# Performance work log

Hardware: AMD Instinct MI355X
Metric: run time of the kernel (lower is better)

## Reference

```python
import jax, jax.numpy as jnp
import numpy as np

N = 30000
NUM_FEAT = 129   # data.x.shape[1] + 1
NUM_CLASSES = 40
HID = 64

def _gat_conv(x, src, dst, W, a_src, a_dst, bias):
    """PyG GATConv (concat=True, negative_slope=0.2), self-loops pre-added to src/dst."""
    n = x.shape[0]
    H, C = a_src.shape
    h = (x @ W).reshape(n, H, C)                       # [N,H,C]
    alpha_s = jnp.sum(h * a_src[None], axis=-1)        # [N,H]
    alpha_d = jnp.sum(h * a_dst[None], axis=-1)        # [N,H]
    e = jax.nn.leaky_relu(alpha_s[src] + alpha_d[dst], 0.2)   # [E,H]
    m = jax.ops.segment_max(e, dst, num_segments=n)
    m = jnp.where(jnp.isfinite(m), m, 0.0)
    ex = jnp.exp(e - m[dst])
    denom = jax.ops.segment_sum(ex, dst, num_segments=n)
    alpha = ex / (denom[dst] + 1e-16)                  # segment softmax over in-edges
    out = jax.ops.segment_sum(h[src] * alpha[:, :, None], dst, num_segments=n)
    return out.reshape(n, H * C) + bias


def setup_inputs() -> dict:
    key = jax.random.key(0)
    ks = jax.random.split(key, 16)
    E = 480000
    x = jax.random.normal(ks[0], (N, NUM_FEAT), dtype=jnp.float32)
    edge_index = jax.random.randint(ks[1], (2, E), 0, N, dtype=jnp.int64)
    def w(k, shape, fan_in):
        return (jax.random.normal(k, shape, dtype=jnp.float32) * (1.0 / np.sqrt(fan_in))).astype(jnp.float32)
    # conv1: in=129, H=7, C=64
    W1 = w(ks[2], (NUM_FEAT, 7 * HID), NUM_FEAT)
    a1s = w(ks[3], (7, HID), HID); a1d = w(ks[4], (7, HID), HID)
    b1 = jnp.zeros((7 * HID,), jnp.float32)
    # conv2: in=448, H=6, C=64
    W2 = w(ks[5], (7 * HID, 6 * HID), 7 * HID)
    a2s = w(ks[6], (6, HID), HID); a2d = w(ks[7], (6, HID), HID)
    b2 = jnp.zeros((6 * HID,), jnp.float32)
    # conv3: in=384, H=6, C=40
    W3 = w(ks[8], (6 * HID, 6 * NUM_CLASSES), 6 * HID)
    a3s = w(ks[9], (6, NUM_CLASSES), NUM_CLASSES); a3d = w(ks[10], (6, NUM_CLASSES), NUM_CLASSES)
    b3 = jnp.zeros((6 * NUM_CLASSES,), jnp.float32)
    return {"x": x, "edge_index": edge_index,
            "W1": W1, "a1s": a1s, "a1d": a1d, "b1": b1,
            "W2": W2, "a2s": a2s, "a2d": a2d, "b2": b2,
            "W3": W3, "a3s": a3s, "a3d": a3d, "b3": b3}


def reference(x, edge_index, W1, a1s, a1d, b1, W2, a2s, a2d, b2, W3, a3s, a3d, b3):
    n = x.shape[0]
    loop = jnp.arange(n, dtype=edge_index.dtype)
    src = jnp.concatenate([edge_index[0], loop])   # PyG add_self_loops=True
    dst = jnp.concatenate([edge_index[1], loop])
    # dropout is identity in eval mode
    h = _gat_conv(x, src, dst, W1, a1s, a1d, b1)
    h = jax.nn.relu(h)
    h = _gat_conv(h, src, dst, W2, a2s, a2d, b2)
    h = jax.nn.relu(h)
    out = _gat_conv(h, src, dst, W3, a3s, a3d, b3)
    return out
```

## Files before the change

kernel.cpp:

```cpp
#include <hip/hip_runtime.h>
#include <hip/hip_bf16.h>


#define NFEAT 129
#define MPAD  30080
#define BLKSH 11
#define KPD   16

typedef __attribute__((ext_vector_type(8))) short short8v;
typedef __attribute__((ext_vector_type(8))) unsigned short u16x8;
typedef __attribute__((ext_vector_type(8))) __bf16 bf16x8;
typedef __attribute__((ext_vector_type(4))) float f32x4;
typedef unsigned short u16;

union FragU { short8v s; bf16x8 b; };

__device__ inline u16 f2bf(float x) {
    unsigned u = __builtin_bit_cast(unsigned, x);
    unsigned r = (u + 0x7fffu + ((u >> 16) & 1u)) >> 16;
    return (u16)r;
}
__device__ inline float bf2f(u16 b) {
    unsigned u = ((unsigned)b) << 16;
    return __builtin_bit_cast(float, u);
}
__device__ inline float h2f(u16 u) { return (float)__builtin_bit_cast(_Float16, u); }
__device__ inline u16 f2h(float v) { return __builtin_bit_cast(u16, (_Float16)v); }


__global__ __launch_bounds__(256) void hist_k(const int* __restrict__ src,
                                              const int* __restrict__ dst,
                                              int* __restrict__ cnt, int E, int n) {
    int e = blockIdx.x * 256 + threadIdx.x;
    if (e < E + n) {
        int s, d;
        if (e < E) { s = src[e]; d = dst[e]; }
        else       { s = d = e - E; }
        atomicAdd(&cnt[d * KPD + (s >> BLKSH)], 1);
    }
}

__global__ __launch_bounds__(256) void bsum_k(const int* __restrict__ cnt,
                                              int* __restrict__ bsum, int nk) {
    __shared__ int sh[256];
    int t = threadIdx.x, idx = blockIdx.x * 256 + t;
    sh[t] = (idx < nk) ? cnt[idx] : 0;
    __syncthreads();
    for (int o = 128; o; o >>= 1) {
        if (t < o) sh[t] += sh[t + o];
        __syncthreads();
    }
    if (t == 0) bsum[blockIdx.x] = sh[0];
}

__global__ __launch_bounds__(1024) void bscan_k(const int* __restrict__ bsum,
                                                int* __restrict__ bofs, int nb) {
    __shared__ int part[1024];
    int t = threadIdx.x;
    int per = (nb + 1023) >> 10;
    int base = t * per;
    int s = 0;
    for (int j = 0; j < per; ++j) {
        int i = base + j;
        if (i < nb) s += bsum[i];
    }
    part[t] = s;
    __syncthreads();
    for (int o = 1; o < 1024; o <<= 1) {
        int v = 0;
        if (t >= o) v = part[t - o];
        __syncthreads();
        if (t >= o) part[t] += v;
        __syncthreads();
    }
    int run = (t > 0) ? part[t - 1] : 0;
    for (int j = 0; j < per; ++j) {
        int i = base + j;
        if (i < nb) { bofs[i] = run; run += bsum[i]; }
    }
    if (t == 1023) bofs[nb] = part[1023];
}

__global__ __launch_bounds__(256) void scanw_k(const int* __restrict__ cnt,
                                               const int* __restrict__ bofs,
                                               int* __restrict__ row_ptr, int nk) {
    __shared__ int sh[256];
    int t = threadIdx.x, idx = blockIdx.x * 256 + t;
    int v = (idx < nk) ? cnt[idx] : 0;
    sh[t] = v;
    __syncthreads();
    for (int o = 1; o < 256; o <<= 1) {
        int u = 0;
        if (t >= o) u = sh[t - o];
        __syncthreads();
        if (t >= o) sh[t] += u;
        __syncthreads();
    }
    if (idx < nk) row_ptr[idx] = bofs[blockIdx.x] + sh[t] - v;
    if (idx == nk - 1) row_ptr[nk] = bofs[blockIdx.x] + sh[t];
}

__global__ __launch_bounds__(256) void scatter_k(const int* __restrict__ src, const int* __restrict__ dst,
                                                 const int* __restrict__ row_ptr, int* __restrict__ fill,
                                                 int* __restrict__ col, int E, int n) {
    int e = blockIdx.x * 256 + threadIdx.x;
    if (e < E + n) {
        int s, d;
        if (e < E) { s = src[e]; d = dst[e]; }
        else       { s = d = e - E; }
        int key = d * KPD + (s >> BLKSH);
        int pos = row_ptr[key] + atomicAdd(&fill[key], 1);
        col[pos] = s;
    }
}


__global__ __launch_bounds__(256) void xsplit_k(const float* __restrict__ in,
                                                u16* __restrict__ hi, u16* __restrict__ lo,
                                                int Nn, int K, int Kp, int Mp) {
    int idx = blockIdx.x * 256 + threadIdx.x;
    if (idx >= Mp * Kp) return;
    int m = idx / Kp, k = idx - m * Kp;
    float v = (m < Nn && k < K) ? in[(size_t)m * K + k] : 0.f;
    u16 h = f2bf(v);
    hi[idx] = h;
    lo[idx] = f2bf(v - bf2f(h));
}


__global__ __launch_bounds__(256) void wsplitAll_k(const float* __restrict__ W1,
                                                   const float* __restrict__ W2,
                                                   const float* __restrict__ W3,
                                                   u16* __restrict__ hi, u16* __restrict__ lo) {
    int idx = blockIdx.x * 256 + threadIdx.x;
    if (idx >= 352256) return;
    const float* W; int loc, Kp, K, N;
    if (idx < 81920)       { W = W1; loc = idx;          Kp = 160; K = 129; N = 448; }
    else if (idx < 253952) { W = W2; loc = idx - 81920;  Kp = 448; K = 448; N = 384; }
    else                   { W = W3; loc = idx - 253952; Kp = 384; K = 384; N = 240; }
    int nn = loc / Kp, k = loc - nn * Kp;
    float v = (k < K && nn < N) ? W[(size_t)k * N + nn] : 0.f;
    u16 h = f2bf(v);
    hi[idx] = h;
    lo[idx] = f2bf(v - bf2f(h));
}


__global__ __launch_bounds__(256) void projAll_k(
    const float* __restrict__ W1, const float* __restrict__ a1s, const float* __restrict__ a1d,
    const float* __restrict__ W2, const float* __restrict__ a2s, const float* __restrict__ a2d,
    const float* __restrict__ W3, const float* __restrict__ a3s, const float* __restrict__ a3d,
    float* __restrict__ Ps, float* __restrict__ Pd) {
    int idx = blockIdx.x * 256 + threadIdx.x;
    if (idx >= 992 * 8) return;
    int row = idx >> 3, h = idx & 7;
    const float *W, *as_, *ad_; int k, K, Ncols, H, C;
    if (row < 160)      { k = row;       K = 129; W = W1; as_ = a1s; ad_ = a1d; Ncols = 448; H = 7; C = 64; }
    else if (row < 608) { k = row - 160; K = 448; W = W2; as_ = a2s; ad_ = a2d; Ncols = 384; H = 6; C = 64; }
    else                { k = row - 608; K = 384; W = W3; as_ = a3s; ad_ = a3d; Ncols = 240; H = 6; C = 40; }
    float ps = 0.f, pd = 0.f;
    if (h < H && k < K) {
        const float* wr = W + (size_t)k * Ncols + h * C;
        const float* ar = as_ + h * C;
        const float* dr = ad_ + h * C;
        for (int c = 0; c < C; ++c) {
            float wv = wr[c];
            ps += wv * ar[c];
            pd += wv * dr[c];
        }
    }
    Ps[idx] = ps;
    Pd[idx] = pd;
}


__global__ __launch_bounds__(256) void zeropads_k(u16* __restrict__ h1hi, u16* __restrict__ h1lo,
                                                  int Nn) {
    int tot = (MPAD - Nn) * 448;
    int idx = blockIdx.x * 256 + threadIdx.x;
    if (idx < tot) {
        h1hi[(size_t)Nn * 448 + idx] = 0;
        h1lo[(size_t)Nn * 448 + idx] = 0;
    }
}


__global__ __launch_bounds__(256) void alpha1_k(const float* __restrict__ x,
                                                const float* __restrict__ Ps,
                                                const float* __restrict__ Pd,
                                                float* __restrict__ oS, float* __restrict__ oD, int n) {
    int wv = threadIdx.x >> 6, lane = threadIdx.x & 63;
    int i = blockIdx.x * 4 + wv;
    if (i >= n) return;
    const float* row = x + (size_t)i * NFEAT;
    float x0 = row[lane], x1 = row[64 + lane];
    float ps[8], pd[8];
    #pragma unroll
    for (int h = 0; h < 8; ++h) {
        ps[h] = x0 * Ps[lane * 8 + h] + x1 * Ps[(64 + lane) * 8 + h];
        pd[h] = x0 * Pd[lane * 8 + h] + x1 * Pd[(64 + lane) * 8 + h];
    }
    if (lane == 0) {
        float x2 = row[128];
        #pragma unroll
        for (int h = 0; h < 8; ++h) {
            ps[h] += x2 * Ps[128 * 8 + h];
            pd[h] += x2 * Pd[128 * 8 + h];
        }
    }
    #pragma unroll
    for (int h = 0; h < 8; ++h) {
        #pragma unroll
        for (int off = 32; off; off >>= 1) {
            ps[h] += __shfl_xor(ps[h], off);
            pd[h] += __shfl_xor(pd[h], off);
        }
    }
    if (lane == 0) {
        #pragma unroll
        for (int h = 0; h < 8; ++h) {
            oS[(size_t)i * 8 + h] = ps[h];
            oD[(size_t)i * 8 + h] = pd[h];
        }
    }
}


__device__ __forceinline__ int swz(int r, int s) {
    return (r << 2) | ((s ^ (r & 3) ^ ((r >> 2) & 3)) & 3);
}


__global__ __launch_bounds__(256) void gemm16(
    const u16* __restrict__ Ahi, const u16* __restrict__ Alo,
    const u16* __restrict__ Bhi, const u16* __restrict__ Blo,
    u16* __restrict__ C16, int M, int Ncols, int Kp)
{
    __shared__ __align__(16) u16 sAh[128 * 32];
    __shared__ __align__(16) u16 sAl[128 * 32];
    __shared__ __align__(16) u16 sBh[128 * 32];
    __shared__ __align__(16) u16 sBl[128 * 32];
    const int tid = threadIdx.x;
    const int m0 = blockIdx.y * 128;
    const int n0 = blockIdx.x * 128;
    const int lane = tid & 63, wave = tid >> 6;
    const int wm = wave >> 1, wn = wave & 1;
    const int l15 = lane & 15, lg = lane >> 4;
    const int r0 = tid >> 2, s0 = tid & 3;
    const int w0 = swz(r0, s0), w1 = swz(r0 + 64, s0);
    f32x4 acc[4][4] = {};

    for (int k0 = 0; k0 < Kp; k0 += 32) {
        size_t gA0 = (size_t)(m0 + r0) * Kp + k0 + s0 * 8;
        size_t gA1 = (size_t)(m0 + r0 + 64) * Kp + k0 + s0 * 8;
        size_t gB0 = (size_t)(n0 + r0) * Kp + k0 + s0 * 8;
        size_t gB1 = (size_t)(n0 + r0 + 64) * Kp + k0 + s0 * 8;
        short8v ah0 = *(const short8v*)(Ahi + gA0);
        short8v ah1 = *(const short8v*)(Ahi + gA1);
        short8v al0 = *(const short8v*)(Alo + gA0);
        short8v al1 = *(const short8v*)(Alo + gA1);
        short8v bh0 = *(const short8v*)(Bhi + gB0);
        short8v bh1 = *(const short8v*)(Bhi + gB1);
        short8v bl0 = *(const short8v*)(Blo + gB0);
        short8v bl1 = *(const short8v*)(Blo + gB1);
        __syncthreads();
        ((short8v*)sAh)[w0] = ah0; ((short8v*)sAh)[w1] = ah1;
        ((short8v*)sAl)[w0] = al0; ((short8v*)sAl)[w1] = al1;
        ((short8v*)sBh)[w0] = bh0; ((short8v*)sBh)[w1] = bh1;
        ((short8v*)sBl)[w0] = bl0; ((short8v*)sBl)[w1] = bl1;
        __syncthreads();
        FragU fah[4], fal[4], fbh[4], fbl[4];
        #pragma unroll
        for (int mf = 0; mf < 4; ++mf) {
            int rr = wm * 64 + mf * 16 + l15;
            int idx = swz(rr, lg);
            fah[mf].s = ((const short8v*)sAh)[idx];
            fal[mf].s = ((const short8v*)sAl)[idx];
        }
        #pragma unroll
        for (int nf = 0; nf < 4; ++nf) {
            int rr = wn * 64 + nf * 16 + l15;
            int idx = swz(rr, lg);
            fbh[nf].s = ((const short8v*)sBh)[idx];
            fbl[nf].s = ((const short8v*)sBl)[idx];
        }
        #pragma unroll
        for (int mf = 0; mf < 4; ++mf) {
            #pragma unroll
            for (int nf = 0; nf < 4; ++nf) {
                acc[mf][nf] = __builtin_amdgcn_mfma_f32_16x16x32_bf16(fah[mf].b, fbh[nf].b, acc[mf][nf], 0, 0, 0);
                acc[mf][nf] = __builtin_amdgcn_mfma_f32_16x16x32_bf16(fah[mf].b, fbl[nf].b, acc[mf][nf], 0, 0, 0);
                acc[mf][nf] = __builtin_amdgcn_mfma_f32_16x16x32_bf16(fal[mf].b, fbh[nf].b, acc[mf][nf], 0, 0, 0);
            }
        }
    }
    #pragma unroll
    for (int mf = 0; mf < 4; ++mf) {
        #pragma unroll
        for (int nf = 0; nf < 4; ++nf) {
            int colg = n0 + wn * 64 + nf * 16 + l15;
            if (colg >= Ncols) continue;
            #pragma unroll
            for (int r = 0; r < 4; ++r) {
                int rowg = m0 + wm * 64 + mf * 16 + lg * 4 + r;
                if (rowg < M) C16[(size_t)rowg * Ncols + colg] = f2h(acc[mf][nf][r]);
            }
        }
    }
}


template <int H, int C, bool RELU, bool SPLIT, bool PROJ>
__global__ __launch_bounds__(256) void aggF_k(
    const u16* __restrict__ hf,
    const float* __restrict__ as_, const float* __restrict__ ad_,
    const float* __restrict__ bias,
    const int* __restrict__ row_ptr,
    const int* __restrict__ col,
    const float* __restrict__ Pns, const float* __restrict__ Pnd,
    float* __restrict__ nas, float* __restrict__ nad,
    float* __restrict__ outf, u16* __restrict__ ohi, u16* __restrict__ olo,
    int n)
{
    constexpr int HC = H * C;
    constexpr int LACT = HC / 8;
    const int wv = threadIdx.x >> 6, lane = threadIdx.x & 63;
    const int i = blockIdx.x * 4 + wv;
    if (i >= n) return;
    const int ch0 = lane * 8;
    const bool act = lane < LACT;
    const int h = act ? (ch0 / C) : 0;
    const bool lead = act && ((ch0 % C) == 0);
    const int beg = row_ptr[i * KPD], end = row_ptr[(i + 1) * KPD];
    float acc[8] = {};
    float dp = 0.f;
    if (act) {
        const float adh = ad_[(size_t)i * 8 + h];
        int e = beg;
        for (; e + 4 <= end; e += 4) {
            int sA = col[e],     sB = col[e + 1];
            int sC = col[e + 2], sD = col[e + 3];
            float fA = as_[(size_t)sA * 8 + h] + adh;
            float fB = as_[(size_t)sB * 8 + h] + adh;
            float fC = as_[(size_t)sC * 8 + h] + adh;
            float fD = as_[(size_t)sD * 8 + h] + adh;
            u16x8 vA = *(const u16x8*)(hf + (size_t)sA * HC + ch0);
            u16x8 vB = *(const u16x8*)(hf + (size_t)sB * HC + ch0);
            u16x8 vC = *(const u16x8*)(hf + (size_t)sC * HC + ch0);
            u16x8 vD = *(const u16x8*)(hf + (size_t)sD * HC + ch0);
            fA = fA > 0.f ? fA : 0.2f * fA;
            fB = fB > 0.f ? fB : 0.2f * fB;
            fC = fC > 0.f ? fC : 0.2f * fC;
            fD = fD > 0.f ? fD : 0.2f * fD;
            float wA = __expf(fA), wB = __expf(fB);
            float wC = __expf(fC), wD = __expf(fD);
            #pragma unroll
            for (int j = 0; j < 8; ++j)
                acc[j] += wA * h2f(vA[j]) + wB * h2f(vB[j])
                        + wC * h2f(vC[j]) + wD * h2f(vD[j]);
            if (lead) dp += (wA + wB) + (wC + wD);
        }
        for (; e + 2 <= end; e += 2) {
            int sA = col[e], sB = col[e + 1];
            float fA = as_[(size_t)sA * 8 + h] + adh;
            float fB = as_[(size_t)sB * 8 + h] + adh;
            u16x8 vA = *(const u16x8*)(hf + (size_t)sA * HC + ch0);
            u16x8 vB = *(const u16x8*)(hf + (size_t)sB * HC + ch0);
            fA = fA > 0.f ? fA : 0.2f * fA;
            fB = fB > 0.f ? fB : 0.2f * fB;
            float wA = __expf(fA), wB = __expf(fB);
            #pragma unroll
            for (int j = 0; j < 8; ++j)
                acc[j] += wA * h2f(vA[j]) + wB * h2f(vB[j]);
            if (lead) dp += wA + wB;
        }
        if (e < end) {
            int sA = col[e];
            float fA = as_[(size_t)sA * 8 + h] + adh;
            u16x8 vA = *(const u16x8*)(hf + (size_t)sA * HC + ch0);
            fA = fA > 0.f ? fA : 0.2f * fA;
            float wA = __expf(fA);
            #pragma unroll
            for (int j = 0; j < 8; ++j)
                acc[j] += wA * h2f(vA[j]);
            if (lead) dp += wA;
        }
    }
    const float den = __shfl(dp, h * (C / 8)) + 1e-16f;
    float o[8];
    #pragma unroll
    for (int j = 0; j < 8; ++j) o[j] = 0.f;
    if (act) {
        #pragma unroll
        for (int j = 0; j < 8; ++j) {
            float v = acc[j] / den + bias[ch0 + j];
            if (RELU) v = fmaxf(v, 0.f);
            o[j] = v;
        }
        size_t base = (size_t)i * HC + ch0;
        if constexpr (SPLIT) {
            u16x8 ph, pl;
            #pragma unroll
            for (int j = 0; j < 8; ++j) {
                u16 hi = f2bf(o[j]);
                ph[j] = hi;
                pl[j] = f2bf(o[j] - bf2f(hi));
            }
            *(u16x8*)(ohi + base) = ph;
            *(u16x8*)(olo + base) = pl;
        } else {
            float4 q0; q0.x = o[0]; q0.y = o[1]; q0.z = o[2]; q0.w = o[3];
            float4 q1; q1.x = o[4]; q1.y = o[5]; q1.z = o[6]; q1.w = o[7];
            *(float4*)(outf + base) = q0;
            *(float4*)(outf + base + 4) = q1;
        }
    }
    if constexpr (PROJ) {
        float ps[8] = {}, pd[8] = {};
        if (act) {
            #pragma unroll
            for (int j = 0; j < 8; ++j) {
                const float* prs = Pns + (size_t)(ch0 + j) * 8;
                const float* prd = Pnd + (size_t)(ch0 + j) * 8;
                #pragma unroll
                for (int hp = 0; hp < 8; ++hp) {
                    ps[hp] += o[j] * prs[hp];
                    pd[hp] += o[j] * prd[hp];
                }
            }
        }
        #pragma unroll
        for (int hp = 0; hp < 8; ++hp) {
            #pragma unroll
            for (int off = 32; off; off >>= 1) {
                ps[hp] += __shfl_xor(ps[hp], off);
                pd[hp] += __shfl_xor(pd[hp], off);
            }
        }
        if (lane == 0) {
            #pragma unroll
            for (int hp = 0; hp < 8; ++hp) {
                nas[(size_t)i * 8 + hp] = ps[hp];
                nad[(size_t)i * 8 + hp] = pd[hp];
            }
        }
    }
}


extern "C" void kernel_launch(void* const* d_in, const int* in_sizes, int n_in,
                              void* d_out, int out_size, void* d_ws, size_t ws_size,
                              hipStream_t stream) {
    const float* x   = (const float*)d_in[0];
    const int*   ei  = (const int*)d_in[1];
    const float* W1  = (const float*)d_in[2];
    const float* a1s = (const float*)d_in[3];
    const float* a1d = (const float*)d_in[4];
    const float* b1  = (const float*)d_in[5];
    const float* W2  = (const float*)d_in[6];
    const float* a2s = (const float*)d_in[7];
    const float* a2d = (const float*)d_in[8];
    const float* b2  = (const float*)d_in[9];
    const float* W3  = (const float*)d_in[10];
    const float* a3s = (const float*)d_in[11];
    const float* a3d = (const float*)d_in[12];
    const float* b3  = (const float*)d_in[13];
    float* out = (float*)d_out;

    const int Nn = in_sizes[0] / NFEAT;
    const int E  = in_sizes[1] / 2;
    const int Et = E + Nn;
    const int NK = Nn * KPD;
    const int NB = (NK + 255) / 256;
    const int* srcp = ei;
    const int* dstp = ei + E;

    char* ws = (char*)d_ws;
    size_t off = 0;
    auto carve = [&](size_t bytes) -> char* {
        char* p = ws + off;
        off += (bytes + 255) & ~(size_t)255;
        return p;
    };
    u16*   hbuf16 = (u16*)carve((size_t)MPAD * 448 * 2);
    u16*   h1hi  = (u16*)carve((size_t)MPAD * 448 * 2);
    u16*   h1lo  = (u16*)carve((size_t)MPAD * 448 * 2);
    u16*   Xhi   = (u16*)carve((size_t)MPAD * 160 * 2);
    u16*   Xlo   = (u16*)carve((size_t)MPAD * 160 * 2);
    u16*   Wthi  = (u16*)carve((size_t)352256 * 2);
    u16*   Wtlo  = (u16*)carve((size_t)352256 * 2);
    int*   col   = (int*)carve((size_t)Et * 4);
    int* row_ptr = (int*)carve((size_t)(NK + 1) * 4);
    int*   cnt   = (int*)carve((size_t)NK * 4);
    int*   bsum  = (int*)carve((size_t)NB * 4);
    int*   bofs  = (int*)carve((size_t)(NB + 1) * 4);
    float* aA    = (float*)carve((size_t)Nn * 8 * 4);
    float* dA    = (float*)carve((size_t)Nn * 8 * 4);
    float* aB    = (float*)carve((size_t)Nn * 8 * 4);
    float* dB    = (float*)carve((size_t)Nn * 8 * 4);
    float* Ps    = (float*)carve((size_t)992 * 8 * 4);
    float* Pd    = (float*)carve((size_t)992 * 8 * 4);
    (void)ws_size;

    const int nb4 = (Nn + 3) / 4;
    const int mg  = MPAD / 128;

    hipMemsetAsync(cnt, 0, (size_t)NK * 4, stream);
    hist_k<<<(Et + 255) / 256, 256, 0, stream>>>(srcp, dstp, cnt, E, Nn);
    bsum_k<<<NB, 256, 0, stream>>>(cnt, bsum, NK);
    bscan_k<<<1, 1024, 0, stream>>>(bsum, bofs, NB);
    scanw_k<<<NB, 256, 0, stream>>>(cnt, bofs, row_ptr, NK);
    hipMemsetAsync(cnt, 0, (size_t)NK * 4, stream);
    scatter_k<<<(Et + 255) / 256, 256, 0, stream>>>(srcp, dstp, row_ptr, cnt, col, E, Nn);

    xsplit_k<<<((MPAD * 160) + 255) / 256, 256, 0, stream>>>(x, Xhi, Xlo, Nn, NFEAT, 160, MPAD);
    wsplitAll_k<<<(352256 + 255) / 256, 256, 0, stream>>>(W1, W2, W3, Wthi, Wtlo);
    projAll_k<<<(992 * 8 + 255) / 256, 256, 0, stream>>>(W1, a1s, a1d, W2, a2s, a2d, W3, a3s, a3d, Ps, Pd);
    zeropads_k<<<(((MPAD - Nn) * 448) + 255) / 256, 256, 0, stream>>>(h1hi, h1lo, Nn);

    alpha1_k<<<nb4, 256, 0, stream>>>(x, Ps, Pd, aA, dA, Nn);
    gemm16<<<dim3(4, mg), 256, 0, stream>>>(Xhi, Xlo, Wthi, Wtlo, hbuf16, Nn, 448, 160);
    aggF_k<7, 64, true, true, true><<<nb4, 256, 0, stream>>>(
        hbuf16, aA, dA, b1, row_ptr, col, Ps + 1280, Pd + 1280, aB, dB,
        nullptr, h1hi, h1lo, Nn);

    gemm16<<<dim3(3, mg), 256, 0, stream>>>(h1hi, h1lo, Wthi + 81920, Wtlo + 81920, hbuf16, Nn, 384, 448);
    aggF_k<6, 64, true, true, true><<<nb4, 256, 0, stream>>>(
        hbuf16, aB, dB, b2, row_ptr, col, Ps + 4864, Pd + 4864, aA, dA,
        nullptr, h1hi, h1lo, Nn);

    gemm16<<<dim3(2, mg), 256, 0, stream>>>(h1hi, h1lo, Wthi + 253952, Wtlo + 253952, hbuf16, Nn, 240, 384);
    aggF_k<6, 40, false, false, false><<<nb4, 256, 0, stream>>>(
        hbuf16, aA, dA, b3, row_ptr, col, nullptr, nullptr, nullptr, nullptr,
        out, nullptr, nullptr, Nn);
}
```

Baseline: 557.7 us.

## Precompute edge weights, store fp32 features, and split aggregation across channel blocks

Adds a per-edge kernel that computes exp(leaky_relu(alpha_s+alpha_d)) for every edge and head into a buffer, using a destination array recorded during the CSR scatter. The GEMM now writes fp32 instead of fp16, and the aggregation reads float4 features over a 2D grid split by channel block. The next layer's attention projection moves out of the aggregation into a separate kernel. This removes redundant exp and gather work per channel lane, but doubles feature gather bytes and adds extra kernels and buffer traffic.

```diff
diff --git a/kernel.cpp b/kernel.cpp
--- a/kernel.cpp
+++ b/kernel.cpp
@@ -24,8 +24,6 @@
     unsigned u = ((unsigned)b) << 16;
     return __builtin_bit_cast(float, u);
 }
-__device__ inline float h2f(u16 u) { return (float)__builtin_bit_cast(_Float16, u); }
-__device__ inline u16 f2h(float v) { return __builtin_bit_cast(u16, (_Float16)v); }
 
 
 __global__ __launch_bounds__(256) void hist_k(const int* __restrict__ src,
@@ -102,7 +100,8 @@
 
 __global__ __launch_bounds__(256) void scatter_k(const int* __restrict__ src, const int* __restrict__ dst,
                                                  const int* __restrict__ row_ptr, int* __restrict__ fill,
-                                                 int* __restrict__ col, int E, int n) {
+                                                 int* __restrict__ col, int* __restrict__ dstc,
+                                                 int E, int n) {
     int e = blockIdx.x * 256 + threadIdx.x;
     if (e < E + n) {
         int s, d;
@@ -111,6 +110,7 @@
         int key = d * KPD + (s >> BLKSH);
         int pos = row_ptr[key] + atomicAdd(&fill[key], 1);
         col[pos] = s;
+        dstc[pos] = d;
     }
 }
 
@@ -226,15 +226,71 @@
 }
 
 
+template <int KC>
+__global__ __launch_bounds__(256) void alphaproj_k(const u16* __restrict__ Hhi,
+                                                   const u16* __restrict__ Hlo,
+                                                   const float* __restrict__ Ps,
+                                                   const float* __restrict__ Pd,
+                                                   float* __restrict__ oS, float* __restrict__ oD, int n) {
+    constexpr int STRIDE = KC * 64;
+    int wv = threadIdx.x >> 6, lane = threadIdx.x & 63;
+    int i = blockIdx.x * 4 + wv;
+    if (i >= n) return;
+    const u16* bh = Hhi + (size_t)i * STRIDE;
+    const u16* bl = Hlo + (size_t)i * STRIDE;
+    float ps[8] = {}, pd[8] = {};
+    #pragma unroll
+    for (int kc = 0; kc < KC; ++kc) {
+        int k = kc * 64 + lane;
+        float v = bf2f(bh[k]) + bf2f(bl[k]);
+        #pragma unroll
+        for (int h = 0; h < 8; ++h) {
+            ps[h] += v * Ps[k * 8 + h];
+            pd[h] += v * Pd[k * 8 + h];
+        }
+    }
+    #pragma unroll
+    for (int h = 0; h < 8; ++h) {
+        #pragma unroll
+        for (int off = 32; off; off >>= 1) {
+            ps[h] += __shfl_xor(ps[h], off);
+            pd[h] += __shfl_xor(pd[h], off);
+        }
+    }
+    if (lane == 0) {
+        #pragma unroll
+        for (int h = 0; h < 8; ++h) {
+            oS[(size_t)i * 8 + h] = ps[h];
+            oD[(size_t)i * 8 + h] = pd[h];
+        }
+    }
+}
+
+
+__global__ __launch_bounds__(256) void edgew_k(const float* __restrict__ as_,
+                                               const float* __restrict__ ad_,
+                                               const int* __restrict__ col,
+                                               const int* __restrict__ dstc,
+                                               float* __restrict__ w, int Et) {
+    int idx = blockIdx.x * 256 + threadIdx.x;
+    if (idx >= Et * 8) return;
+    int e = idx >> 3, h = idx & 7;
+    int s = col[e], d = dstc[e];
+    float v = as_[(size_t)s * 8 + h] + ad_[(size_t)d * 8 + h];
+    v = v > 0.f ? v : 0.2f * v;
+    w[idx] = __expf(v);
+}
+
+
 __device__ __forceinline__ int swz(int r, int s) {
     return (r << 2) | ((s ^ (r & 3) ^ ((r >> 2) & 3)) & 3);
 }
 
 
-__global__ __launch_bounds__(256) void gemm16(
+__global__ __launch_bounds__(256) void gemm32(
     const u16* __restrict__ Ahi, const u16* __restrict__ Alo,
     const u16* __restrict__ Bhi, const u16* __restrict__ Blo,
-    u16* __restrict__ C16, int M, int Ncols, int Kp)
+    float* __restrict__ C, int M, int Ncols, int Kp)
 {
     __shared__ __align__(16) u16 sAh[128 * 32];
     __shared__ __align__(16) u16 sAl[128 * 32];
@@ -303,146 +359,76 @@
             #pragma unroll
             for (int r = 0; r < 4; ++r) {
                 int rowg = m0 + wm * 64 + mf * 16 + lg * 4 + r;
-                if (rowg < M) C16[(size_t)rowg * Ncols + colg] = f2h(acc[mf][nf][r]);
+                if (rowg < M) C[(size_t)rowg * Ncols + colg] = acc[mf][nf][r];
             }
         }
     }
 }
 
 
-template <int H, int C, bool RELU, bool SPLIT, bool PROJ>
-__global__ __launch_bounds__(256) void aggF_k(
-    const u16* __restrict__ hf,
-    const float* __restrict__ as_, const float* __restrict__ ad_,
+template <int H, int C, int CPB, bool RELU, bool SPLIT>
+__global__ __launch_bounds__(256) void gat_agg4(
+    const float* __restrict__ hfeat, const float* __restrict__ w,
     const float* __restrict__ bias,
-    const int* __restrict__ row_ptr,
-    const int* __restrict__ col,
-    const float* __restrict__ Pns, const float* __restrict__ Pnd,
-    float* __restrict__ nas, float* __restrict__ nad,
-    float* __restrict__ outf, u16* __restrict__ ohi, u16* __restrict__ olo,
-    int n)
+    const int* __restrict__ row_ptr, const int* __restrict__ col,
+    float* __restrict__ outf, u16* __restrict__ ohi, u16* __restrict__ olo, int n)
 {
     constexpr int HC = H * C;
-    constexpr int LACT = HC / 8;
     const int wv = threadIdx.x >> 6, lane = threadIdx.x & 63;
     const int i = blockIdx.x * 4 + wv;
     if (i >= n) return;
-    const int ch0 = lane * 8;
-    const bool act = lane < LACT;
-    const int h = act ? (ch0 / C) : 0;
-    const bool lead = act && ((ch0 % C) == 0);
+    const int ch = blockIdx.y * CPB + lane * 4;
+    const bool act = (lane * 4 < CPB) && (ch < HC);
+    const int h = act ? (ch / C) : 0;
+    const int cinh = act ? (ch % C) : 0;
     const int beg = row_ptr[i * KPD], end = row_ptr[(i + 1) * KPD];
-    float acc[8] = {};
-    float dp = 0.f;
+    float a0 = 0.f, a1 = 0.f, a2 = 0.f, a3 = 0.f, dp = 0.f;
     if (act) {
-        const float adh = ad_[(size_t)i * 8 + h];
+        const bool lead = (cinh == 0);
         int e = beg;
-        for (; e + 4 <= end; e += 4) {
-            int sA = col[e],     sB = col[e + 1];
-            int sC = col[e + 2], sD = col[e + 3];
-            float fA = as_[(size_t)sA * 8 + h] + adh;
-            float fB = as_[(size_t)sB * 8 + h] + adh;
-            float fC = as_[(size_t)sC * 8 + h] + adh;
-            float fD = as_[(size_t)sD * 8 + h] + adh;
-            u16x8 vA = *(const u16x8*)(hf + (size_t)sA * HC + ch0);
-            u16x8 vB = *(const u16x8*)(hf + (size_t)sB * HC + ch0);
-            u16x8 vC = *(const u16x8*)(hf + (size_t)sC * HC + ch0);
-            u16x8 vD = *(const u16x8*)(hf + (size_t)sD * HC + ch0);
-            fA = fA > 0.f ? fA : 0.2f * fA;
-            fB = fB > 0.f ? fB : 0.2f * fB;
-            fC = fC > 0.f ? fC : 0.2f * fC;
-            fD = fD > 0.f ? fD : 0.2f * fD;
-            float wA = __expf(fA), wB = __expf(fB);
-            float wC = __expf(fC), wD = __expf(fD);
-            #pragma unroll
-            for (int j = 0; j < 8; ++j)
-                acc[j] += wA * h2f(vA[j]) + wB * h2f(vB[j])
-                        + wC * h2f(vC[j]) + wD * h2f(vD[j]);
-            if (lead) dp += (wA + wB) + (wC + wD);
-        }
         for (; e + 2 <= end; e += 2) {
             int sA = col[e], sB = col[e + 1];
-            float fA = as_[(size_t)sA * 8 + h] + adh;
-            float fB = as_[(size_t)sB * 8 + h] + adh;
-            u16x8 vA = *(const u16x8*)(hf + (size_t)sA * HC + ch0);
-            u16x8 vB = *(const u16x8*)(hf + (size_t)sB * HC + ch0);
-            fA = fA > 0.f ? fA : 0.2f * fA;
-            fB = fB > 0.f ? fB : 0.2f * fB;
-            float wA = __expf(fA), wB = __expf(fB);
-            #pragma unroll
-            for (int j = 0; j < 8; ++j)
-                acc[j] += wA * h2f(vA[j]) + wB * h2f(vB[j]);
+            float wA = w[(size_t)e * 8 + h];
+            float wB = w[(size_t)(e + 1) * 8 + h];
+            float4 hA = *(const float4*)(hfeat + (size_t)sA * HC + ch);
+            float4 hB = *(const float4*)(hfeat + (size_t)sB * HC + ch);
+            a0 += wA * hA.x + wB * hB.x;
+            a1 += wA * hA.y + wB * hB.y;
+            a2 += wA * hA.z + wB * hB.z;
+            a3 += wA * hA.w + wB * hB.w;
             if (lead) dp += wA + wB;
         }
         if (e < end) {
             int sA = col[e];
-            float fA = as_[(size_t)sA * 8 + h] + adh;
-            u16x8 vA = *(const u16x8*)(hf + (size_t)sA * HC + ch0);
-            fA = fA > 0.f ? fA : 0.2f * fA;
-            float wA = __expf(fA);
-            #pragma unroll
-            for (int j = 0; j < 8; ++j)
-                acc[j] += wA * h2f(vA[j]);
+            float wA = w[(size_t)e * 8 + h];
+            float4 hA = *(const float4*)(hfeat + (size_t)sA * HC + ch);
+            a0 += wA * hA.x; a1 += wA * hA.y; a2 += wA * hA.z; a3 += wA * hA.w;
             if (lead) dp += wA;
         }
     }
-    const float den = __shfl(dp, h * (C / 8)) + 1e-16f;
-    float o[8];
-    #pragma unroll
-    for (int j = 0; j < 8; ++j) o[j] = 0.f;
+    const float den = __shfl(dp, lane - (cinh >> 2)) + 1e-16f;
     if (act) {
-        #pragma unroll
-        for (int j = 0; j < 8; ++j) {
-            float v = acc[j] / den + bias[ch0 + j];
-            if (RELU) v = fmaxf(v, 0.f);
-            o[j] = v;
-        }
-        size_t base = (size_t)i * HC + ch0;
+        const float4 b4 = *(const float4*)(bias + ch);
+        float o0 = a0 / den + b4.x;
+        float o1 = a1 / den + b4.y;
+        float o2 = a2 / den + b4.z;
+        float o3 = a3 / den + b4.w;
+        if (RELU) {
+            o0 = fmaxf(o0, 0.f); o1 = fmaxf(o1, 0.f);
+            o2 = fmaxf(o2, 0.f); o3 = fmaxf(o3, 0.f);
+        }
+        size_t base = (size_t)i * HC + ch;
         if constexpr (SPLIT) {
-            u16x8 ph, pl;
-            #pragma unroll
-            for (int j = 0; j < 8; ++j) {
-                u16 hi = f2bf(o[j]);
-                ph[j] = hi;
-                pl[j] = f2bf(o[j] - bf2f(hi));
-            }
-            *(u16x8*)(ohi + base) = ph;
-            *(u16x8*)(olo + base) = pl;
+            ushort4 ph, pl;
+            ph.x = f2bf(o0); pl.x = f2bf(o0 - bf2f(ph.x));
+            ph.y = f2bf(o1); pl.y = f2bf(o1 - bf2f(ph.y));
+            ph.z = f2bf(o2); pl.z = f2bf(o2 - bf2f(ph.z));
+            ph.w = f2bf(o3); pl.w = f2bf(o3 - bf2f(ph.w));
+            *(ushort4*)(ohi + base) = ph;
+            *(ushort4*)(olo + base) = pl;
         } else {
-            float4 q0; q0.x = o[0]; q0.y = o[1]; q0.z = o[2]; q0.w = o[3];
-            float4 q1; q1.x = o[4]; q1.y = o[5]; q1.z = o[6]; q1.w = o[7];
-            *(float4*)(outf + base) = q0;
-            *(float4*)(outf + base + 4) = q1;
-        }
-    }
-    if constexpr (PROJ) {
-        float ps[8] = {}, pd[8] = {};
-        if (act) {
-            #pragma unroll
-            for (int j = 0; j < 8; ++j) {
-                const float* prs = Pns + (size_t)(ch0 + j) * 8;
-                const float* prd = Pnd + (size_t)(ch0 + j) * 8;
-                #pragma unroll
-                for (int hp = 0; hp < 8; ++hp) {
-                    ps[hp] += o[j] * prs[hp];
-                    pd[hp] += o[j] * prd[hp];
-                }
-            }
-        }
-        #pragma unroll
-        for (int hp = 0; hp < 8; ++hp) {
-            #pragma unroll
-            for (int off = 32; off; off >>= 1) {
-                ps[hp] += __shfl_xor(ps[hp], off);
-                pd[hp] += __shfl_xor(pd[hp], off);
-            }
-        }
-        if (lane == 0) {
-            #pragma unroll
-            for (int hp = 0; hp < 8; ++hp) {
-                nas[(size_t)i * 8 + hp] = ps[hp];
-                nad[(size_t)i * 8 + hp] = pd[hp];
-            }
+            float4 o; o.x = o0; o.y = o1; o.z = o2; o.w = o3;
+            *(float4*)(outf + base) = o;
         }
     }
 }
@@ -482,14 +468,16 @@
         off += (bytes + 255) & ~(size_t)255;
         return p;
     };
-    u16*   hbuf16 = (u16*)carve((size_t)MPAD * 448 * 2);
+    float* hbuf  = (float*)carve((size_t)MPAD * 448 * 4);
     u16*   h1hi  = (u16*)carve((size_t)MPAD * 448 * 2);
     u16*   h1lo  = (u16*)carve((size_t)MPAD * 448 * 2);
     u16*   Xhi   = (u16*)carve((size_t)MPAD * 160 * 2);
     u16*   Xlo   = (u16*)carve((size_t)MPAD * 160 * 2);
     u16*   Wthi  = (u16*)carve((size_t)352256 * 2);
     u16*   Wtlo  = (u16*)carve((size_t)352256 * 2);
+    float* wbuf  = (float*)carve((size_t)Et * 8 * 4);
     int*   col   = (int*)carve((size_t)Et * 4);
+    int*   dstc  = (int*)carve((size_t)Et * 4);
     int* row_ptr = (int*)carve((size_t)(NK + 1) * 4);
     int*   cnt   = (int*)carve((size_t)NK * 4);
     int*   bsum  = (int*)carve((size_t)NB * 4);
@@ -511,7 +499,7 @@
     bscan_k<<<1, 1024, 0, stream>>>(bsum, bofs, NB);
     scanw_k<<<NB, 256, 0, stream>>>(cnt, bofs, row_ptr, NK);
     hipMemsetAsync(cnt, 0, (size_t)NK * 4, stream);
-    scatter_k<<<(Et + 255) / 256, 256, 0, stream>>>(srcp, dstp, row_ptr, cnt, col, E, Nn);
+    scatter_k<<<(Et + 255) / 256, 256, 0, stream>>>(srcp, dstp, row_ptr, cnt, col, dstc, E, Nn);
 
     xsplit_k<<<((MPAD * 160) + 255) / 256, 256, 0, stream>>>(x, Xhi, Xlo, Nn, NFEAT, 160, MPAD);
     wsplitAll_k<<<(352256 + 255) / 256, 256, 0, stream>>>(W1, W2, W3, Wthi, Wtlo);
@@ -519,18 +507,20 @@
     zeropads_k<<<(((MPAD - Nn) * 448) + 255) / 256, 256, 0, stream>>>(h1hi, h1lo, Nn);
 
     alpha1_k<<<nb4, 256, 0, stream>>>(x, Ps, Pd, aA, dA, Nn);
-    gemm16<<<dim3(4, mg), 256, 0, stream>>>(Xhi, Xlo, Wthi, Wtlo, hbuf16, Nn, 448, 160);
-    aggF_k<7, 64, true, true, true><<<nb4, 256, 0, stream>>>(
-        hbuf16, aA, dA, b1, row_ptr, col, Ps + 1280, Pd + 1280, aB, dB,
-        nullptr, h1hi, h1lo, Nn);
-
-    gemm16<<<dim3(3, mg), 256, 0, stream>>>(h1hi, h1lo, Wthi + 81920, Wtlo + 81920, hbuf16, Nn, 384, 448);
-    aggF_k<6, 64, true, true, true><<<nb4, 256, 0, stream>>>(
-        hbuf16, aB, dB, b2, row_ptr, col, Ps + 4864, Pd + 4864, aA, dA,
-        nullptr, h1hi, h1lo, Nn);
-
-    gemm16<<<dim3(2, mg), 256, 0, stream>>>(h1hi, h1lo, Wthi + 253952, Wtlo + 253952, hbuf16, Nn, 240, 384);
-    aggF_k<6, 40, false, false, false><<<nb4, 256, 0, stream>>>(
-        hbuf16, aA, dA, b3, row_ptr, col, nullptr, nullptr, nullptr, nullptr,
-        out, nullptr, nullptr, Nn);
-}
+    edgew_k<<<(Et * 8 + 255) / 256, 256, 0, stream>>>(aA, dA, col, dstc, wbuf, Et);
+    gemm32<<<dim3(4, mg), 256, 0, stream>>>(Xhi, Xlo, Wthi, Wtlo, hbuf, Nn, 448, 160);
+    gat_agg4<7, 64, 256, true, true><<<dim3(nb4, 2), 256, 0, stream>>>(
+        hbuf, wbuf, b1, row_ptr, col, nullptr, h1hi, h1lo, Nn);
+    alphaproj_k<7><<<nb4, 256, 0, stream>>>(h1hi, h1lo, Ps + 1280, Pd + 1280, aB, dB, Nn);
+
+    edgew_k<<<(Et * 8 + 255) / 256, 256, 0, stream>>>(aB, dB, col, dstc, wbuf, Et);
+    gemm32<<<dim3(3, mg), 256, 0, stream>>>(h1hi, h1lo, Wthi + 81920, Wtlo + 81920, hbuf, Nn, 384, 448);
+    gat_agg4<6, 64, 192, true, true><<<dim3(nb4, 2), 256, 0, stream>>>(
+        hbuf, wbuf, b2, row_ptr, col, nullptr, h1hi, h1lo, Nn);
+    alphaproj_k<6><<<nb4, 256, 0, stream>>>(h1hi, h1lo, Ps + 4864, Pd + 4864, aA, dA, Nn);
+
+    edgew_k<<<(Et * 8 + 255) / 256, 256, 0, stream>>>(aA, dA, col, dstc, wbuf, Et);
+    gemm32<<<dim3(2, mg), 256, 0, stream>>>(h1hi, h1lo, Wthi + 253952, Wtlo + 253952, hbuf, Nn, 240, 384);
+    gat_agg4<6, 40, 240, false, false><<<dim3(nb4, 1), 256, 0, stream>>>(
+        hbuf, wbuf, b3, row_ptr, col, out, nullptr, nullptr, Nn);
+}
```

Result: slower. 634.3 us (+13.7%).
